# Performance work log

Hardware: AMD Instinct MI355X
Metric: run time of the kernel (lower is better)

The kernel has to match this reference:

```python
import jax, jax.numpy as jnp
import numpy as np

NUM_CLASSES = 100000
FEAT_DIM = 128
BATCH = 1024
CLAMP_MIN = 1e-12
CLAMP_MAX = 1e12


def setup_inputs() -> dict:
    key = jax.random.key(0)
    k1, k2, k3 = jax.random.split(key, 3)
    input_x = jax.random.normal(k1, (BATCH, FEAT_DIM), dtype=jnp.float32)
    input_label = jax.random.randint(k2, (BATCH,), 0, NUM_CLASSES, dtype=jnp.int64)
    # learned parameter: class centers, initialized ~N(0,1) as in the module
    centers = jax.random.normal(k3, (NUM_CLASSES, FEAT_DIM), dtype=jnp.float32)
    return {"input_x": input_x, "input_label": input_label, "centers": centers}


def reference(input_x, input_label, centers):
    # distmat[b, c] = ||x_b||^2 + ||center_c||^2 - 2 <x_b, center_c>   -> [B, C]
    x_sq = jnp.sum(input_x * input_x, axis=1, keepdims=True)          # [B, 1]
    c_sq = jnp.sum(centers * centers, axis=1)[None, :]                # [1, C]
    distmat = x_sq + c_sq - 2.0 * (input_x @ centers.T)               # [B, C]
    # mask selects the true-class column per sample
    mask = (input_label[:, None] == jnp.arange(NUM_CLASSES)[None, :]).astype(distmat.dtype)
    dist = distmat * mask
    # NOTE: faithful to the original — clamp is applied AFTER masking, so every
    # masked-off zero entry clamps up to 1e-12 and contributes to the sum.
    loss = jnp.clip(dist, CLAMP_MIN, CLAMP_MAX).sum() / BATCH
    return loss
```

## Files before the change

kernel.cpp:

```cpp
#include <hip/hip_runtime.h>


#define BATCH 1024
#define FEAT_DIM 128
#define NUM_CLASSES 100000
#define NBLK 64

__global__ __launch_bounds__(256) void center_loss_main(
        const float* __restrict__ x,
        const int* __restrict__ label,
        const float* __restrict__ centers,
        float* __restrict__ out,
        unsigned int* __restrict__ counter,
        float* __restrict__ partials) {
    const int lane = threadIdx.x & 63;
    const int wid  = threadIdx.x >> 6;

    const int base = blockIdx.x * 16 + wid * 4;
    float wsum = 0.f;
    #pragma unroll
    for (int r = 0; r < 4; ++r) {
        const int row = base + r;
        const int lbl = label[row];
        const float2 xv = *reinterpret_cast<const float2*>(x + (size_t)row * FEAT_DIM + lane * 2);
        const float2 cv = *reinterpret_cast<const float2*>(centers + (size_t)lbl * FEAT_DIM + lane * 2);
        const float d0 = xv.x - cv.x;
        const float d1 = xv.y - cv.y;
        float s = d0 * d0 + d1 * d1;
        #pragma unroll
        for (int off = 32; off > 0; off >>= 1)
            s += __shfl_xor(s, off, 64);
        wsum += fminf(fmaxf(s, 1e-12f), 1e12f);
    }

    __shared__ float sm[4];
    __shared__ int is_last;
    if (lane == 0) sm[wid] = wsum;
    __syncthreads();
    if (threadIdx.x == 0) {
        const float bsum = (sm[0] + sm[1]) + (sm[2] + sm[3]);
        __hip_atomic_store(&partials[blockIdx.x], bsum,
                           __ATOMIC_RELEASE, __HIP_MEMORY_SCOPE_AGENT);
        const unsigned old = __hip_atomic_fetch_add(counter, 1u,
                           __ATOMIC_ACQ_REL, __HIP_MEMORY_SCOPE_AGENT);
        is_last = (old == NBLK - 1) ? 1 : 0;
    }
    __syncthreads();

    if (is_last && wid == 0) {
        float v = __hip_atomic_load(&partials[lane],
                                    __ATOMIC_ACQUIRE, __HIP_MEMORY_SCOPE_AGENT);
        #pragma unroll
        for (int off = 32; off > 0; off >>= 1)
            v += __shfl_xor(v, off, 64);
        if (lane == 0) {
            out[0] = v * (1.0f / (float)BATCH) + (float)(NUM_CLASSES - 1) * 1e-12f;
            __hip_atomic_store(counter, 0u,
                               __ATOMIC_RELAXED, __HIP_MEMORY_SCOPE_AGENT);
        }
    }
}

extern "C" void kernel_launch(void* const* d_in, const int* in_sizes, int n_in,
                              void* d_out, int out_size, void* d_ws, size_t ws_size,
                              hipStream_t stream) {
    const float* x       = (const float*)d_in[0];
    const int*   label   = (const int*)d_in[1];
    const float* centers = (const float*)d_in[2];
    float*       out     = (float*)d_out;

    unsigned int* counter  = (unsigned int*)d_ws;
    float*        partials = (float*)((char*)d_ws + 256);

    hipMemsetAsync(d_ws, 0, 4, stream);
    center_loss_main<<<NBLK, 256, 0, stream>>>(x, label, centers, out, counter, partials);
}
```

Before: 13.93 us.

## Replace atomic last-block reduction with separate finish kernel, drop memset

```diff
diff --git a/kernel.cpp b/kernel.cpp
--- a/kernel.cpp
+++ b/kernel.cpp
@@ -6,24 +6,25 @@
 #define NUM_CLASSES 100000
 #define NBLK 64
 
-__global__ __launch_bounds__(256) void center_loss_main(
+__global__ __launch_bounds__(256) void center_partials(
         const float* __restrict__ x,
         const int* __restrict__ label,
         const float* __restrict__ centers,
-        float* __restrict__ out,
-        unsigned int* __restrict__ counter,
         float* __restrict__ partials) {
     const int lane = threadIdx.x & 63;
     const int wid  = threadIdx.x >> 6;
+    const int base = blockIdx.x * 16 + wid * 4;
 
-    const int base = blockIdx.x * 16 + wid * 4;
+    int lbl[4];
+    #pragma unroll
+    for (int r = 0; r < 4; ++r) lbl[r] = label[base + r];
+
     float wsum = 0.f;
     #pragma unroll
     for (int r = 0; r < 4; ++r) {
         const int row = base + r;
-        const int lbl = label[row];
         const float2 xv = *reinterpret_cast<const float2*>(x + (size_t)row * FEAT_DIM + lane * 2);
-        const float2 cv = *reinterpret_cast<const float2*>(centers + (size_t)lbl * FEAT_DIM + lane * 2);
+        const float2 cv = *reinterpret_cast<const float2*>(centers + (size_t)lbl[r] * FEAT_DIM + lane * 2);
         const float d0 = xv.x - cv.x;
         const float d1 = xv.y - cv.y;
         float s = d0 * d0 + d1 * d1;
@@ -34,30 +35,21 @@
     }
 
     __shared__ float sm[4];
-    __shared__ int is_last;
     if (lane == 0) sm[wid] = wsum;
     __syncthreads();
+    if (threadIdx.x == 0)
+        partials[blockIdx.x] = (sm[0] + sm[1]) + (sm[2] + sm[3]);
+}
+
+__global__ __launch_bounds__(64) void center_finish(
+        const float* __restrict__ partials,
+        float* __restrict__ out) {
+    float v = partials[threadIdx.x & 63];
+    #pragma unroll
+    for (int off = 32; off > 0; off >>= 1)
+        v += __shfl_xor(v, off, 64);
     if (threadIdx.x == 0) {
-        const float bsum = (sm[0] + sm[1]) + (sm[2] + sm[3]);
-        __hip_atomic_store(&partials[blockIdx.x], bsum,
-                           __ATOMIC_RELEASE, __HIP_MEMORY_SCOPE_AGENT);
-        const unsigned old = __hip_atomic_fetch_add(counter, 1u,
-                           __ATOMIC_ACQ_REL, __HIP_MEMORY_SCOPE_AGENT);
-        is_last = (old == NBLK - 1) ? 1 : 0;
-    }
-    __syncthreads();
-
-    if (is_last && wid == 0) {
-        float v = __hip_atomic_load(&partials[lane],
-                                    __ATOMIC_ACQUIRE, __HIP_MEMORY_SCOPE_AGENT);
-        #pragma unroll
-        for (int off = 32; off > 0; off >>= 1)
-            v += __shfl_xor(v, off, 64);
-        if (lane == 0) {
-            out[0] = v * (1.0f / (float)BATCH) + (float)(NUM_CLASSES - 1) * 1e-12f;
-            __hip_atomic_store(counter, 0u,
-                               __ATOMIC_RELAXED, __HIP_MEMORY_SCOPE_AGENT);
-        }
+        out[0] = v * (1.0f / (float)BATCH) + (float)(NUM_CLASSES - 1) * 1e-12f;
     }
 }
 
@@ -68,10 +60,8 @@
     const int*   label   = (const int*)d_in[1];
     const float* centers = (const float*)d_in[2];
     float*       out     = (float*)d_out;
+    float*       ws      = (float*)d_ws;
 
-    unsigned int* counter  = (unsigned int*)d_ws;
-    float*        partials = (float*)((char*)d_ws + 256);
-
-    hipMemsetAsync(d_ws, 0, 4, stream);
-    center_loss_main<<<NBLK, 256, 0, stream>>>(x, label, centers, out, counter, partials);
+    center_partials<<<NBLK, 256, 0, stream>>>(x, label, centers, ws);
+    center_finish<<<1, 64, 0, stream>>>(ws, out);
 }
```

New measurement: 11.33 us (median of 2 runs). -18.7%, faster.
